# Kernel optimization log

Measured on AMD Instinct MI355X. Metric: run time of the kernel, lower is better.

The kernel has to match this reference:

```python
import jax, jax.numpy as jnp
import numpy as np

NE, NR, NT = 100000, 400, 1000000   # entities, relations, triples
B, DH, T = 32, 512, 3               # batch, hidden dim, num_steps
SELF_REL = 0                        # vocab['relation2id']['<SELF_REL>']


def setup_inputs() -> dict:
    key = jax.random.key(0)
    ks = jax.random.split(key, 10)
    questions = jax.random.randint(ks[0], (B, 1), 0, NR)
    e_s = jax.nn.one_hot(jax.random.randint(ks[1], (B,), 0, NE), NE, dtype=jnp.float32)
    answers = jax.nn.one_hot(jax.random.randint(ks[2], (B,), 0, NE), NE, dtype=jnp.float32)
    # KG triples (replaces sparse incidence matrices Msubj/Mrel/Mobj)
    subj_idx = jax.random.randint(ks[3], (NT,), 0, NE)
    rel_idx = jax.random.randint(ks[4], (NT,), 0, NR)
    obj_idx = jax.random.randint(ks[5], (NT,), 0, NE)
    # learned parameters
    rel_emb = jax.random.normal(ks[6], (NR, DH), dtype=jnp.float32) / np.float32(np.sqrt(DH))
    step_W = jax.random.normal(ks[7], (T, DH, DH), dtype=jnp.float32) * np.float32(np.sqrt(2.0 / DH))
    step_b = jnp.zeros((T, DH), dtype=jnp.float32)
    ent_emb = jax.random.normal(ks[8], (NE, DH), dtype=jnp.float32) / np.float32(np.sqrt(DH))
    ent_bias = jnp.zeros((NE,), dtype=jnp.float32)
    return dict(questions=questions, e_s=e_s, answers=answers,
                subj_idx=subj_idx, rel_idx=rel_idx, obj_idx=obj_idx,
                rel_emb=rel_emb, step_W=step_W, step_b=step_b,
                ent_emb=ent_emb, ent_bias=ent_bias)


def _follow(e, r, subj, rel, obj):
    # torch: (Mobj.T @ (Msubj @ e.T * Mrel @ r.T)).T
    x = e[:, subj] * r[:, rel]                 # [B, NT] per-triple message
    return jnp.zeros_like(e).at[:, obj].add(x)  # scatter-add to object entities


def reference(questions, e_s, answers, subj_idx, rel_idx, obj_idx,
              rel_emb, step_W, step_b, ent_emb, ent_bias):
    num_steps = step_W.shape[0]
    q_emb = rel_emb[questions[:, 0]]           # [B, DH]
    last_e = e_s
    rel_probs = []
    ent_probs = [e_s]
    for t in range(num_steps):
        cq_t = jnp.tanh(q_emb @ step_W[t].T + step_b[t])          # step encoder
        rel_dist = jax.nn.softmax(cq_t @ rel_emb.T, axis=1)       # [B, NR]
        last_e = _follow(last_e, rel_dist, subj_idx, rel_idx, obj_idx)
        if t == 0:
            gt = jnp.take_along_axis(rel_dist, questions, axis=1)  # [B,1]
            last_e = last_e - answers * gt
        rel_probs.append(rel_dist)
        # clamp scores > 1 by (detached) self-normalization
        m = (last_e > 1).astype(last_e.dtype)
        z = jax.lax.stop_gradient(m * last_e + (1 - m))
        last_e = last_e / z
        if t > 0:
            prev_rel = jnp.argmax(rel_probs[-2], axis=1)
            curr_rel = jnp.argmax(rel_probs[-1], axis=1)
            cond = (jnp.abs(prev_rel - curr_rel) == 1) & (jnp.minimum(prev_rel, curr_rel) % 2 == 0)
            m2 = cond.astype(last_e.dtype)[:, None]
            ent_m = m2 * (ent_probs[-2] > 0.9).astype(last_e.dtype)
            last_e = (1 - ent_m) * last_e
        if t == num_steps - 1:
            stack_rel = jnp.argmax(jnp.stack(rel_probs, axis=1), axis=2)  # [B, T]
            num_self = jnp.sum((stack_rel == SELF_REL).astype(jnp.int32), axis=1)
            m3 = (num_self == 1).astype(last_e.dtype)[:, None] * e_s
            last_e = (1 - m3) * last_e
        ent_probs.append(jax.lax.stop_gradient(last_e))
    e_score = last_e
    normed = e_score / (jnp.sum(e_score, axis=1, keepdims=True) + 1e-6)
    pred_e = (jax.lax.stop_gradient(normed) @ ent_emb) @ ent_emb.T + ent_bias[None, :]
    return e_score, pred_e
```

## Files before the change

### kernel.cpp

```cpp
#include <hip/hip_runtime.h>
#include <math.h>

#define NE 100000
#define NR 400
#define NT 1000000
#define B  32
#define DH 512

__global__ __launch_bounds__(256) void prep_kernel(
    const float* __restrict__ e_s, const float* __restrict__ answers,
    float* __restrict__ E0, float* __restrict__ E1,
    int* __restrict__ SRC, int* __restrict__ ANS)
{
    int bid = blockIdx.x, tid = threadIdx.x;
    __shared__ float tile[32 * 33];
    int base_e = bid * 32;
    #pragma unroll
    for (int l = 0; l < 4; ++l) {
        int idx = l * 256 + tid;
        int br = idx >> 5, ec = idx & 31;
        float v = e_s[(size_t)br * NE + base_e + ec];
        float a = answers[(size_t)br * NE + base_e + ec];
        tile[ec * 33 + br] = v;
        if (v > 0.5f) SRC[br] = base_e + ec;
        if (a > 0.5f) ANS[br] = base_e + ec;
    }
    __syncthreads();
    #pragma unroll
    for (int l = 0; l < 4; ++l) {
        int idx = l * 256 + tid;
        int ew = idx >> 5, bw = idx & 31;
        E0[(size_t)(base_e + ew) * 32 + bw] = tile[ew * 33 + bw];
        E1[(size_t)base_e * 32 + idx] = 0.f;
    }
}

__global__ __launch_bounds__(256) void stepA_kernel(
    int t,
    const int* __restrict__ questions,
    const float* __restrict__ rel_emb,
    const float* __restrict__ step_W,
    const float* __restrict__ step_b,
    float* __restrict__ RD, float* __restrict__ GT,
    int* __restrict__ AM, int* __restrict__ COND, int* __restrict__ FLAG3)
{
    __shared__ float qe[DH];
    __shared__ float cq[DH];
    __shared__ float lg[NR];
    __shared__ float rv[256];
    __shared__ int   ri[256];
    int b = blockIdx.x, tid = threadIdx.x;
    int q = questions[b];

    for (int i = tid; i < DH; i += 256) qe[i] = rel_emb[(size_t)q * DH + i];
    __syncthreads();

    for (int i = tid; i < DH; i += 256) {
        const float4* w4 = (const float4*)(step_W + ((size_t)t * DH + i) * DH);
        float acc = step_b[t * DH + i];
        for (int j = 0; j < DH / 4; ++j) {
            float4 wv = w4[j];
            acc += wv.x * qe[4*j] + wv.y * qe[4*j+1] + wv.z * qe[4*j+2] + wv.w * qe[4*j+3];
        }
        cq[i] = tanhf(acc);
    }
    __syncthreads();

    float lmax = -1e30f; int lidx = 0;
    for (int r = tid; r < NR; r += 256) {
        const float4* re4 = (const float4*)(rel_emb + (size_t)r * DH);
        float acc = 0.f;
        for (int j = 0; j < DH / 4; ++j) {
            float4 wv = re4[j];
            acc += wv.x * cq[4*j] + wv.y * cq[4*j+1] + wv.z * cq[4*j+2] + wv.w * cq[4*j+3];
        }
        lg[r] = acc;
        if (acc > lmax) { lmax = acc; lidx = r; }
    }
    rv[tid] = lmax; ri[tid] = lidx;
    __syncthreads();
    for (int s = 128; s > 0; s >>= 1) {
        if (tid < s) {
            float ov = rv[tid + s]; int oi = ri[tid + s];
            if (ov > rv[tid] || (ov == rv[tid] && oi < ri[tid])) { rv[tid] = ov; ri[tid] = oi; }
        }
        __syncthreads();
    }
    float mx = rv[0]; int amax = ri[0];
    __syncthreads();

    float lsum = 0.f;
    for (int r = tid; r < NR; r += 256) {
        float ex = expf(lg[r] - mx);
        lg[r] = ex;
        lsum += ex;
    }
    rv[tid] = lsum;
    __syncthreads();
    for (int s = 128; s > 0; s >>= 1) {
        if (tid < s) rv[tid] += rv[tid + s];
        __syncthreads();
    }
    float Z = rv[0];

    for (int r = tid; r < NR; r += 256) RD[r * B + b] = lg[r] / Z;

    if (tid == 0) {
        AM[t * B + b] = amax;
        if (t == 0) GT[b] = lg[q] / Z;
        if (t >= 1) {
            int ap = AM[(t - 1) * B + b];
            int d = ap - amax; if (d < 0) d = -d;
            int mn = ap < amax ? ap : amax;
            COND[(t - 1) * B + b] = (d == 1 && (mn % 2 == 0)) ? 1 : 0;
        }
        if (t == 2) {
            int a0 = AM[0 * B + b], a1 = AM[1 * B + b];
            int c = (a0 == 0) + (a1 == 0) + (amax == 0);
            FLAG3[b] = (c == 1) ? 1 : 0;
        }
    }
}

__global__ __launch_bounds__(256) void follow_kernel(
    const float* __restrict__ Ein, float* __restrict__ Eout,
    const float* __restrict__ RD,
    const int* __restrict__ subj, const int* __restrict__ rel,
    const int* __restrict__ obj)
{
    long long gid = (long long)blockIdx.x * 256 + threadIdx.x;
    int trip = (int)(gid >> 5);
    int b = threadIdx.x & 31;
    if (trip < NT) {
        int s = subj[trip];
        float ev = Ein[(size_t)s * 32 + b];
        if (ev != 0.f) {
            int r = rel[trip];
            int o = obj[trip];
            float x = ev * RD[r * B + b];
            if (x != 0.f) unsafeAtomicAdd(&Eout[(size_t)o * 32 + b], x);
        }
    }
}

__global__ __launch_bounds__(256) void post0_kernel(
    float* __restrict__ E1, float* __restrict__ E2,
    const int* __restrict__ ANS, const float* __restrict__ GT)
{
    int idx = blockIdx.x * 256 + threadIdx.x;
    int b = idx & 31, e = idx >> 5;
    float v = E1[idx];
    if (e == ANS[b]) v -= GT[b];
    if (v > 1.f) v = 1.f;
    E1[idx] = v;
    E2[idx] = 0.f;
}

__global__ __launch_bounds__(256) void post1_kernel(
    float* __restrict__ E2, float* __restrict__ E0,
    const int* __restrict__ COND1, const int* __restrict__ SRC,
    float* __restrict__ P, float* __restrict__ S, int* __restrict__ CNT)
{
    int idx = blockIdx.x * 256 + threadIdx.x;
    int b = idx & 31, e = idx >> 5;
    float v = E2[idx];
    if (v > 1.f) v = 1.f;
    if (COND1[b] && e == SRC[b]) v = 0.f;
    E2[idx] = v;
    E0[idx] = 0.f;
    if (idx < B * DH) P[idx] = 0.f;
    if (idx < B)      S[idx] = 0.f;
    if (idx == 0)     CNT[0] = 0;
}

#define POST2_BLOCKS 512
__global__ __launch_bounds__(256) void post2_kernel(
    float* __restrict__ E0, const float* __restrict__ E1,
    const int* __restrict__ COND2, const int* __restrict__ SRC,
    const int* __restrict__ FLAG3, float* __restrict__ S,
    int* __restrict__ LIST, int* __restrict__ CNT)
{
    __shared__ float sS[32];
    __shared__ int   lbuf[200];
    __shared__ int   lcnt;
    __shared__ int   lbase;
    int tid = threadIdx.x;
    int b = tid & 31;
    if (tid < 32) sS[tid] = 0.f;
    if (tid == 0) lcnt = 0;
    __syncthreads();

    int c2 = COND2[b];
    int f3 = FLAG3[b];
    int sr = SRC[b];

    float local = 0.f;
    for (int idx = blockIdx.x * 256 + tid; idx < NE * B; idx += POST2_BLOCKS * 256) {
        int e = idx >> 5;
        float v = E0[idx];
        if (v > 1.f) v = 1.f;
        if (c2 && E1[idx] > 0.9f) v = 0.f;
        if (f3 && e == sr) v = 0.f;
        E0[idx] = v;
        local += v;
        unsigned long long m = __ballot(v != 0.f);
        int lane = tid & 63;
        if (lane == 0 && (unsigned)(m & 0xffffffffULL)) {
            int p = atomicAdd(&lcnt, 1); lbuf[p] = e;
        }
        if (lane == 32 && (unsigned)(m >> 32)) {
            int p = atomicAdd(&lcnt, 1); lbuf[p] = e;
        }
    }
    local += __shfl_xor(local, 32, 64);
    if ((tid & 63) < 32) atomicAdd(&sS[b], local);
    __syncthreads();
    if (tid < 32) unsafeAtomicAdd(&S[tid], sS[tid]);
    if (tid == 0) lbase = atomicAdd(CNT, lcnt);
    __syncthreads();
    for (int i = tid; i < lcnt; i += 256) LIST[lbase + i] = lbuf[i];
}

__global__ __launch_bounds__(256) void outT_kernel(
    const float* __restrict__ E0, float* __restrict__ out0)
{
    __shared__ float tile[32 * 33];
    int bid = blockIdx.x, tid = threadIdx.x;
    int base_e = bid * 32;
    #pragma unroll
    for (int l = 0; l < 4; ++l) {
        int idx = l * 256 + tid;
        int er = idx >> 5, br = idx & 31;
        tile[br * 33 + er] = E0[(size_t)(base_e + er) * 32 + br];
    }
    __syncthreads();
    #pragma unroll
    for (int l = 0; l < 4; ++l) {
        int idx = l * 256 + tid;
        int bw = idx >> 5, ew = idx & 31;
        out0[(size_t)bw * NE + base_e + ew] = tile[bw * 33 + ew];
    }
}

#define G1_LC 128
#define G1_BLOCKS (G1_LC * 4)

__global__ __launch_bounds__(256) void gemm1_kernel(
    const float* __restrict__ E0, const float* __restrict__ emb,
    const int* __restrict__ LIST, const int* __restrict__ CNT,
    float* __restrict__ PPART)
{
    int tid = threadIdx.x;
    int dc  = blockIdx.x & 3;
    int lc  = blockIdx.x >> 2;
    int bg  = tid >> 6;
    int dl  = tid & 63;
    int cnt = CNT[0];
    const float2* emb2 = (const float2*)emb;
    int off2 = dc * 64 + dl;

    float2 acc[8];
    #pragma unroll
    for (int k = 0; k < 8; ++k) { acc[k].x = 0.f; acc[k].y = 0.f; }

#define G1_FMA(Wv, Ev, kk) \
    acc[kk+0].x += Ev.x * Wv.x; acc[kk+0].y += Ev.x * Wv.y; \
    acc[kk+1].x += Ev.y * Wv.x; acc[kk+1].y += Ev.y * Wv.y; \
    acc[kk+2].x += Ev.z * Wv.x; acc[kk+2].y += Ev.z * Wv.y; \
    acc[kk+3].x += Ev.w * Wv.x; acc[kk+3].y += Ev.w * Wv.y;

    int i = lc;
    for (; i + G1_LC < cnt; i += 2 * G1_LC) {
        int ei0 = LIST[i];
        int ei1 = LIST[i + G1_LC];
        float2 w0 = emb2[(size_t)ei0 * 256 + off2];
        float4 a0 = *(const float4*)(E0 + (size_t)ei0 * 32 + bg * 8);
        float4 b0 = *(const float4*)(E0 + (size_t)ei0 * 32 + bg * 8 + 4);
        float2 w1 = emb2[(size_t)ei1 * 256 + off2];
        float4 a1 = *(const float4*)(E0 + (size_t)ei1 * 32 + bg * 8);
        float4 b1 = *(const float4*)(E0 + (size_t)ei1 * 32 + bg * 8 + 4);
        G1_FMA(w0, a0, 0) G1_FMA(w0, b0, 4)
        G1_FMA(w1, a1, 0) G1_FMA(w1, b1, 4)
    }
    if (i < cnt) {
        int ei0 = LIST[i];
        float2 w0 = emb2[(size_t)ei0 * 256 + off2];
        float4 a0 = *(const float4*)(E0 + (size_t)ei0 * 32 + bg * 8);
        float4 b0 = *(const float4*)(E0 + (size_t)ei0 * 32 + bg * 8 + 4);
        G1_FMA(w0, a0, 0) G1_FMA(w0, b0, 4)
    }
#undef G1_FMA

    float* pp = PPART + ((size_t)lc * 32 + bg * 8) * DH + dc * 128 + dl * 2;
    #pragma unroll
    for (int k = 0; k < 8; ++k) *(float2*)(pp + (size_t)k * DH) = acc[k];
}

__global__ __launch_bounds__(256) void reduceP_kernel(
    const float* __restrict__ PPART, float* __restrict__ P)
{
    int j = blockIdx.x * 256 + threadIdx.x;
    const float4* pp = (const float4*)PPART;
    float4 s; s.x = s.y = s.z = s.w = 0.f;
    for (int lc = 0; lc < G1_LC; ++lc) {
        float4 v = pp[(size_t)lc * (B * DH / 4) + j];
        s.x += v.x; s.y += v.y; s.z += v.z; s.w += v.w;
    }
    ((float4*)P)[j] = s;
}

__global__ __launch_bounds__(256) void gemm2_kernel(
    const float* __restrict__ P, const float* __restrict__ S,
    const float* __restrict__ emb, const float* __restrict__ bias,
    float* __restrict__ out1)
{
    __shared__ float pl[B * DH];
    int tid = threadIdx.x;
    for (int k = tid; k < B * DH; k += 256) {
        int b = k >> 9;
        pl[k] = P[k] / (S[b] + 1e-6f);
    }
    __syncthreads();

    int base = blockIdx.x * 512;
    int e0 = base + tid, e1 = base + 256 + tid;
    int g0 = e0 < NE ? e0 : NE - 1;
    int g1 = e1 < NE ? e1 : NE - 1;
    const float4* emb4 = (const float4*)emb;
    const float4* pl4  = (const float4*)pl;

    float acc0[32], acc1[32];
    #pragma unroll
    for (int b = 0; b < 32; ++b) { acc0[b] = 0.f; acc1[b] = 0.f; }

    for (int dg = 0; dg < 128; ++dg) {
        float4 w0 = emb4[(size_t)g0 * 128 + dg];
        float4 w1 = emb4[(size_t)g1 * 128 + dg];
        #pragma unroll
        for (int b = 0; b < 32; ++b) {
            float4 pv = pl4[b * 128 + dg];
            acc0[b] += w0.x * pv.x + w0.y * pv.y + w0.z * pv.z + w0.w * pv.w;
            acc1[b] += w1.x * pv.x + w1.y * pv.y + w1.z * pv.z + w1.w * pv.w;
        }
    }
    float b0 = bias[g0], b1 = bias[g1];
    #pragma unroll
    for (int b = 0; b < 32; ++b) {
        if (e0 < NE) out1[(size_t)b * NE + e0] = acc0[b] + b0;
        if (e1 < NE) out1[(size_t)b * NE + e1] = acc1[b] + b1;
    }
}

extern "C" void kernel_launch(void* const* d_in, const int* in_sizes, int n_in,
                              void* d_out, int out_size, void* d_ws, size_t ws_size,
                              hipStream_t stream)
{
    const int*   questions = (const int*)d_in[0];
    const float* e_s       = (const float*)d_in[1];
    const float* answers   = (const float*)d_in[2];
    const int*   subj      = (const int*)d_in[3];
    const int*   rel       = (const int*)d_in[4];
    const int*   obj       = (const int*)d_in[5];
    const float* rel_emb   = (const float*)d_in[6];
    const float* step_W    = (const float*)d_in[7];
    const float* step_b    = (const float*)d_in[8];
    const float* ent_emb   = (const float*)d_in[9];
    const float* ent_bias  = (const float*)d_in[10];

    float* out0 = (float*)d_out;
    float* out1 = out0 + (size_t)B * NE;

    float* w  = (float*)d_ws;
    float* E0 = w;
    float* E1 = E0 + (size_t)NE * B;
    float* E2 = E1 + (size_t)NE * B;
    float* RD = E2 + (size_t)NE * B;
    float* P  = RD + NR * B;
    float* S  = P + B * DH;
    float* GT = S + B;
    int* AM    = (int*)(GT + B);
    int* COND  = AM + 3 * B;
    int* FLAG3 = COND + 2 * B;
    int* SRC   = FLAG3 + B;
    int* ANS   = SRC + B;
    int* LIST  = ANS + B;
    int* CNT   = LIST + NE;
    float* PPART = E2;

    const int postGrid = NE * B / 256;

    prep_kernel<<<NE / 32, 256, 0, stream>>>(e_s, answers, E0, E1, SRC, ANS);

    stepA_kernel<<<B, 256, 0, stream>>>(0, questions, rel_emb, step_W, step_b,
                                        RD, GT, AM, COND, FLAG3);
    follow_kernel<<<NT * 32 / 256, 256, 0, stream>>>(E0, E1, RD, subj, rel, obj);
    post0_kernel<<<postGrid, 256, 0, stream>>>(E1, E2, ANS, GT);

    stepA_kernel<<<B, 256, 0, stream>>>(1, questions, rel_emb, step_W, step_b,
                                        RD, GT, AM, COND, FLAG3);
    follow_kernel<<<NT * 32 / 256, 256, 0, stream>>>(E1, E2, RD, subj, rel, obj);
    post1_kernel<<<postGrid, 256, 0, stream>>>(E2, E0, COND, SRC, P, S, CNT);

    stepA_kernel<<<B, 256, 0, stream>>>(2, questions, rel_emb, step_W, step_b,
                                        RD, GT, AM, COND, FLAG3);
    follow_kernel<<<NT * 32 / 256, 256, 0, stream>>>(E2, E0, RD, subj, rel, obj);
    post2_kernel<<<POST2_BLOCKS, 256, 0, stream>>>(E0, E1, COND + B, SRC, FLAG3,
                                                   S, LIST, CNT);

    outT_kernel<<<NE / 32, 256, 0, stream>>>(E0, out0);
    gemm1_kernel<<<G1_BLOCKS, 256, 0, stream>>>(E0, ent_emb, LIST, CNT, PPART);
    reduceP_kernel<<<B * DH / 4 / 256, 256, 0, stream>>>(PPART, P);
    gemm2_kernel<<<(NE + 511) / 512, 256, 0, stream>>>(P, S, ent_emb, ent_bias, out1);
}
```

Before: 863.8 us.

## Fold normalization into reduceP and split gemm2 over batch halves without LDS

The per-row normalization by S moves from gemm2 into reduceP, so gemm2 no longer loads and scales a 64KB shared-memory copy of P in every block. gemm2 now gives each thread one entity and 16 batch rows, with a 2D grid splitting the batch into halves. It reads P straight from global memory through the cache. This cuts the accumulator count from 64 to 16 per thread and drops the large LDS allocation, which should raise occupancy. The cost is that each embedding row is read twice, once per batch half, and P is read from global or L2 instead of LDS. The now-unused zeroing of P in post1 is also removed.

```diff
diff --git a/kernel.cpp b/kernel.cpp
--- a/kernel.cpp
+++ b/kernel.cpp
@@ -159,7 +159,7 @@
 __global__ __launch_bounds__(256) void post1_kernel(
     float* __restrict__ E2, float* __restrict__ E0,
     const int* __restrict__ COND1, const int* __restrict__ SRC,
-    float* __restrict__ P, float* __restrict__ S, int* __restrict__ CNT)
+    float* __restrict__ S, int* __restrict__ CNT)
 {
     int idx = blockIdx.x * 256 + threadIdx.x;
     int b = idx & 31, e = idx >> 5;
@@ -168,7 +168,6 @@
     if (COND1[b] && e == SRC[b]) v = 0.f;
     E2[idx] = v;
     E0[idx] = 0.f;
-    if (idx < B * DH) P[idx] = 0.f;
     if (idx < B)      S[idx] = 0.f;
     if (idx == 0)     CNT[0] = 0;
 }
@@ -297,57 +296,52 @@
 }
 
 __global__ __launch_bounds__(256) void reduceP_kernel(
-    const float* __restrict__ PPART, float* __restrict__ P)
+    const float* __restrict__ PPART, const float* __restrict__ S,
+    float* __restrict__ P)
 {
     int j = blockIdx.x * 256 + threadIdx.x;
+    int b = j >> 7;
     const float4* pp = (const float4*)PPART;
     float4 s; s.x = s.y = s.z = s.w = 0.f;
     for (int lc = 0; lc < G1_LC; ++lc) {
         float4 v = pp[(size_t)lc * (B * DH / 4) + j];
         s.x += v.x; s.y += v.y; s.z += v.z; s.w += v.w;
     }
+    float inv = 1.f / (S[b] + 1e-6f);
+    s.x *= inv; s.y *= inv; s.z *= inv; s.w *= inv;
     ((float4*)P)[j] = s;
 }
 
+#define G2_EPB 256
 __global__ __launch_bounds__(256) void gemm2_kernel(
-    const float* __restrict__ P, const float* __restrict__ S,
+    const float* __restrict__ Pn,
     const float* __restrict__ emb, const float* __restrict__ bias,
     float* __restrict__ out1)
 {
-    __shared__ float pl[B * DH];
     int tid = threadIdx.x;
-    for (int k = tid; k < B * DH; k += 256) {
-        int b = k >> 9;
-        pl[k] = P[k] / (S[b] + 1e-6f);
-    }
-    __syncthreads();
-
-    int base = blockIdx.x * 512;
-    int e0 = base + tid, e1 = base + 256 + tid;
-    int g0 = e0 < NE ? e0 : NE - 1;
-    int g1 = e1 < NE ? e1 : NE - 1;
-    const float4* emb4 = (const float4*)emb;
-    const float4* pl4  = (const float4*)pl;
-
-    float acc0[32], acc1[32];
-    #pragma unroll
-    for (int b = 0; b < 32; ++b) { acc0[b] = 0.f; acc1[b] = 0.f; }
-
-    for (int dg = 0; dg < 128; ++dg) {
-        float4 w0 = emb4[(size_t)g0 * 128 + dg];
-        float4 w1 = emb4[(size_t)g1 * 128 + dg];
+    int e  = blockIdx.x * G2_EPB + tid;
+    int bh = blockIdx.y * 16;
+    int ge = e < NE ? e : NE - 1;
+    const float4* erow = (const float4*)(emb + (size_t)ge * DH);
+    const float4* prow = (const float4*)(Pn + (size_t)bh * DH);
+
+    float acc[16];
+    #pragma unroll
+    for (int b = 0; b < 16; ++b) acc[b] = 0.f;
+
+    for (int dg = 0; dg < DH / 4; ++dg) {
+        float4 w = erow[dg];
         #pragma unroll
-        for (int b = 0; b < 32; ++b) {
-            float4 pv = pl4[b * 128 + dg];
-            acc0[b] += w0.x * pv.x + w0.y * pv.y + w0.z * pv.z + w0.w * pv.w;
-            acc1[b] += w1.x * pv.x + w1.y * pv.y + w1.z * pv.z + w1.w * pv.w;
-        }
-    }
-    float b0 = bias[g0], b1 = bias[g1];
-    #pragma unroll
-    for (int b = 0; b < 32; ++b) {
-        if (e0 < NE) out1[(size_t)b * NE + e0] = acc0[b] + b0;
-        if (e1 < NE) out1[(size_t)b * NE + e1] = acc1[b] + b1;
+        for (int b = 0; b < 16; ++b) {
+            float4 pv = prow[b * (DH / 4) + dg];
+            acc[b] += w.x * pv.x + w.y * pv.y + w.z * pv.z + w.w * pv.w;
+        }
+    }
+    float bi = bias[ge];
+    if (e < NE) {
+        #pragma unroll
+        for (int b = 0; b < 16; ++b)
+            out1[(size_t)(bh + b) * NE + e] = acc[b] + bi;
     }
 }
 
@@ -399,7 +393,7 @@
     stepA_kernel<<<B, 256, 0, stream>>>(1, questions, rel_emb, step_W, step_b,
                                         RD, GT, AM, COND, FLAG3);
     follow_kernel<<<NT * 32 / 256, 256, 0, stream>>>(E1, E2, RD, subj, rel, obj);
-    post1_kernel<<<postGrid, 256, 0, stream>>>(E2, E0, COND, SRC, P, S, CNT);
+    post1_kernel<<<postGrid, 256, 0, stream>>>(E2, E0, COND, SRC, S, CNT);
 
     stepA_kernel<<<B, 256, 0, stream>>>(2, questions, rel_emb, step_W, step_b,
                                         RD, GT, AM, COND, FLAG3);
@@ -409,6 +403,7 @@
 
     outT_kernel<<<NE / 32, 256, 0, stream>>>(E0, out0);
     gemm1_kernel<<<G1_BLOCKS, 256, 0, stream>>>(E0, ent_emb, LIST, CNT, PPART);
-    reduceP_kernel<<<B * DH / 4 / 256, 256, 0, stream>>>(PPART, P);
-    gemm2_kernel<<<(NE + 511) / 512, 256, 0, stream>>>(P, S, ent_emb, ent_bias, out1);
-}
+    reduceP_kernel<<<B * DH / 4 / 256, 256, 0, stream>>>(PPART, S, P);
+    dim3 g2grid((NE + G2_EPB - 1) / G2_EPB, 2);
+    gemm2_kernel<<<g2grid, 256, 0, stream>>>(P, ent_emb, ent_bias, out1);
+}
```

Result: slower. 1.125 ms (+30.2%).
